# Optimization experiments

Measured on AMD Instinct MI355X. Metric: run time of the kernel, lower is better.

Reference implementation:

```python
import jax, jax.numpy as jnp
import numpy as np

B, S, D = 2, 2048, 1024
H = 16
HD = D // H  # 64
FORESIGHT = -1e9  # masked_fill value for non-causal positions


def setup_inputs() -> dict:
    key = jax.random.key(0)
    ks = jax.random.split(key, 8)
    s = 0.02
    return {
        "x": jax.random.normal(ks[0], (B, S, D), dtype=jnp.float32),
        "Wq": jax.random.normal(ks[1], (D, H * HD), dtype=jnp.float32) * s,
        "bq": jax.random.normal(ks[2], (H * HD,), dtype=jnp.float32) * s,
        "Wk": jax.random.normal(ks[3], (D, H * HD), dtype=jnp.float32) * s,
        "Wv": jax.random.normal(ks[4], (D, H * HD), dtype=jnp.float32) * s,
        "Wo": jax.random.normal(ks[5], (H * HD, D), dtype=jnp.float32) * s,
        "bo": jax.random.normal(ks[6], (D,), dtype=jnp.float32) * s,
    }


def reference(x, Wq, bq, Wk, Wv, Wo, bo):
    b, s, _ = x.shape
    # projections -> [B, H, S, HD]
    q = (x @ Wq + bq).reshape(b, s, H, HD).transpose(0, 2, 1, 3)
    k = (x @ Wk).reshape(b, s, H, HD).transpose(0, 2, 1, 3)
    v = (x @ Wv).reshape(b, s, H, HD).transpose(0, 2, 1, 3)
    # scores [B, H, S, S]
    scores = jnp.einsum("bhqd,bhkd->bhqk", q, k) / jnp.sqrt(jnp.float32(HD))
    # ALiBi bias: slope_h * j (key position), broadcast over queries
    slopes = 2.0 ** (-8.0 * jnp.arange(1, H + 1, dtype=jnp.float32) / H)
    positions = jnp.arange(s, dtype=jnp.float32)
    scores = scores - slopes[None, :, None, None] * positions[None, None, None, :]
    # causal mask: fill strictly-upper triangle with foresight
    causal = jnp.tril(jnp.ones((s, s), dtype=bool))
    scores = jnp.where(causal[None, None, :, :], scores, FORESIGHT)
    attn = jax.nn.softmax(scores, axis=-1)
    out = jnp.einsum("bhqk,bhkd->bhqd", attn, v)
    out = out.transpose(0, 2, 1, 3).reshape(b, s, H * HD)
    return out @ Wo + bo
```

## Files before the change

kernel.cpp:

```cpp
#include <hip/hip_runtime.h>
#include <stdint.h>

#define DDIM 1024
#define HH 16
#define HDIM 64
#define SS 2048

typedef short bf16x8 __attribute__((ext_vector_type(8)));
typedef short bf16x4 __attribute__((ext_vector_type(4)));
typedef float f32x4 __attribute__((ext_vector_type(4)));
typedef unsigned short u16;

__device__ __forceinline__ unsigned f2bf(float f) {
  unsigned u = __builtin_bit_cast(unsigned, f);
  u = u + 0x7FFFu + ((u >> 16) & 1u);
  return u >> 16;
}

__device__ __forceinline__ void mfma16(f32x4& c, bf16x4 a, bf16x4 b) {
  asm("v_mfma_f32_16x16x16_bf16 %0, %1, %2, %0" : "+v"(c) : "v"(a), "v"(b));
}

__device__ __forceinline__ void gload16(const void* g, void* l) {
  __builtin_amdgcn_global_load_lds(
      (const __attribute__((address_space(1))) unsigned int*)g,
      (__attribute__((address_space(3))) unsigned int*)l, 16, 0, 0);
}

__global__ void k_convert_x(const float* __restrict__ x, u16* __restrict__ xb) {
  int i = (blockIdx.x * 256 + threadIdx.x) * 4;
  float4 v = *(const float4*)(x + i);
  ushort4 o;
  o.x = (u16)f2bf(v.x); o.y = (u16)f2bf(v.y); o.z = (u16)f2bf(v.z); o.w = (u16)f2bf(v.w);
  *(ushort4*)(xb + i) = o;
}

__global__ void k_transpose_w(const float* __restrict__ w0, const float* __restrict__ w1,
                              const float* __restrict__ w2, const float* __restrict__ w3,
                              u16* __restrict__ wt) {
  __shared__ float t[64][65];
  int z = blockIdx.z;
  const float* src = (z == 0) ? w0 : (z == 1) ? w1 : (z == 2) ? w2 : w3;
  u16* dst = wt + (size_t)z * DDIM * DDIM;
  int k0 = blockIdx.x * 64, n0 = blockIdx.y * 64;
  int tid = threadIdx.x;
  int c4 = tid & 15, rr = tid >> 4;
  for (int rep = 0; rep < 4; rep++) {
    int r = rr + rep * 16;
    float4 v = *(const float4*)(src + (size_t)(k0 + r) * DDIM + n0 + c4 * 4);
    t[r][c4 * 4 + 0] = v.x; t[r][c4 * 4 + 1] = v.y;
    t[r][c4 * 4 + 2] = v.z; t[r][c4 * 4 + 3] = v.w;
  }
  __syncthreads();
  for (int rep = 0; rep < 4; rep++) {
    int n = rr + rep * 16;
    ushort4 o;
    o.x = (u16)f2bf(t[c4 * 4 + 0][n]); o.y = (u16)f2bf(t[c4 * 4 + 1][n]);
    o.z = (u16)f2bf(t[c4 * 4 + 2][n]); o.w = (u16)f2bf(t[c4 * 4 + 3][n]);
    *(ushort4*)(dst + (size_t)(n0 + n) * DDIM + k0 + c4 * 4) = o;
  }
}

template <int MODE>
__global__ __launch_bounds__(256, 2) void k_gemm(const u16* __restrict__ A,
                                                 const u16* __restrict__ BT,
                                                 const float* __restrict__ bias,
                                                 void* __restrict__ O0,
                                                 void* __restrict__ O1,
                                                 void* __restrict__ O2) {
  __shared__ __align__(16) u16 lA[128 * 64];
  __shared__ __align__(16) u16 lB[128 * 64];
  const int tid = threadIdx.x;
  const int l = tid & 63, w = tid >> 6;
  const int wm = w >> 1, wn = w & 1;
  const int m0 = blockIdx.x * 128, n0 = blockIdx.y * 128;
  const int lr = l >> 4, lc = l & 15;

  const int srow = l >> 3;
  const int scol = ((l & 7) ^ srow) * 8;

  f32x4 acc[4][4];
  for (int mi = 0; mi < 4; mi++)
    for (int ni = 0; ni < 4; ni++)
      acc[mi][ni] = f32x4{0.f, 0.f, 0.f, 0.f};

  for (int kk = 0; kk < 16; kk++) {
    const int k0 = kk * 64;
    for (int i = 0; i < 4; i++) {
      int c = w * 4 + i;
      gload16(A + (size_t)(m0 + c * 8 + srow) * DDIM + k0 + scol, (char*)lA + c * 1024);
      gload16(BT + (size_t)(n0 + c * 8 + srow) * DDIM + k0 + scol, (char*)lB + c * 1024);
    }
    __syncthreads();
    for (int ks = 0; ks < 2; ks++) {
      bf16x8 af[4], bfr[4];
      for (int mi = 0; mi < 4; mi++) {
        int row = wm * 64 + mi * 16 + lc;
        int slot = (ks * 4 + lr) ^ (row & 7);
        af[mi] = *(const bf16x8*)((const char*)lA + row * 128 + slot * 16);
      }
      for (int ni = 0; ni < 4; ni++) {
        int row = wn * 64 + ni * 16 + lc;
        int slot = (ks * 4 + lr) ^ (row & 7);
        bfr[ni] = *(const bf16x8*)((const char*)lB + row * 128 + slot * 16);
      }
      for (int mi = 0; mi < 4; mi++)
        for (int ni = 0; ni < 4; ni++)
          acc[mi][ni] = __builtin_amdgcn_mfma_f32_16x16x32_bf16(af[mi], bfr[ni], acc[mi][ni], 0, 0, 0);
    }
    __syncthreads();
  }

  if (MODE == 0) {
    const int which = blockIdx.y >> 3;
    if (which == 0) {
      u16* C = (u16*)O0;
      for (int mi = 0; mi < 4; mi++)
        for (int ni = 0; ni < 4; ni++) {
          int nl = (n0 + wn * 64 + ni * 16 + lc) & 1023;
          float badd = bias[nl];
          for (int r = 0; r < 4; r++) {
            int m = m0 + wm * 64 + mi * 16 + lr * 4 + r;
            C[(size_t)m * DDIM + nl] = (u16)f2bf(acc[mi][ni][r] + badd);
          }
        }
    } else if (which == 1) {
      u16* C = (u16*)O1;
      for (int mi = 0; mi < 4; mi++)
        for (int ni = 0; ni < 4; ni++) {
          int nl = (n0 + wn * 64 + ni * 16 + lc) & 1023;
          for (int r = 0; r < 4; r++) {
            int m = m0 + wm * 64 + mi * 16 + lr * 4 + r;
            C[(size_t)m * DDIM + nl] = (u16)f2bf(acc[mi][ni][r]);
          }
        }
    } else {
      u16* C = (u16*)O2;
      for (int mi = 0; mi < 4; mi++)
        for (int ni = 0; ni < 4; ni++) {
          int nl = (n0 + wn * 64 + ni * 16 + lc) & 1023;
          int h = nl >> 6, hd = nl & 63;
          int m = m0 + wm * 64 + mi * 16 + lr * 4;
          int b = m >> 11, s = m & 2047;
          unsigned d0 = f2bf(acc[mi][ni][0]) | (f2bf(acc[mi][ni][1]) << 16);
          unsigned d1 = f2bf(acc[mi][ni][2]) | (f2bf(acc[mi][ni][3]) << 16);
          u16* p = C + ((size_t)((b * HH + h) * HDIM + hd)) * SS + s;
          *(unsigned*)(p) = d0;
          *(unsigned*)(p + 2) = d1;
        }
    }
  } else {
    float* C = (float*)O0;
    for (int mi = 0; mi < 4; mi++)
      for (int ni = 0; ni < 4; ni++) {
        int n = n0 + wn * 64 + ni * 16 + lc;
        float badd = bias[n];
        for (int r = 0; r < 4; r++) {
          int m = m0 + wm * 64 + mi * 16 + lr * 4 + r;
          C[(size_t)m * DDIM + n] = acc[mi][ni][r] + badd;
        }
      }
  }
}

__device__ __forceinline__ void attn_tile(int kt, bool masked, int kfhi,
                                          const char* lKc, const char* lVc,
                                          const bf16x8 qf[2], f32x4 of[4],
                                          float& mrun, float& lrun,
                                          float slope, int lr, int lc, int q_glob) {
  f32x4 sf[8];
#pragma unroll
  for (int kf = 0; kf < 8; kf++) sf[kf] = f32x4{0.f, 0.f, 0.f, 0.f};
#pragma unroll
  for (int ks = 0; ks < 2; ks++)
#pragma unroll
    for (int kf = 0; kf < 8; kf++) {
      if (kf >= kfhi) continue;
      int key = kf * 16 + lc;
      int slot = (ks * 4 + lr) ^ (lc & 7);
      bf16x8 a = *(const bf16x8*)(lKc + key * 128 + slot * 16);
      sf[kf] = __builtin_amdgcn_mfma_f32_16x16x32_bf16(a, qf[ks], sf[kf], 0, 0, 0);
    }

  float tmax = -INFINITY;
#pragma unroll
  for (int kf = 0; kf < 8; kf++) {
    if (kf >= kfhi) continue;
#pragma unroll
    for (int r = 0; r < 4; r++) {
      int key = kt * 128 + kf * 16 + lr * 4 + r;
      float sv = sf[kf][r] * 0.125f - slope * (float)key;
      if (masked && key > q_glob) sv = -1e9f;
      sf[kf][r] = sv;
      tmax = fmaxf(tmax, sv);
    }
  }
  tmax = fmaxf(tmax, __shfl_xor(tmax, 16));
  tmax = fmaxf(tmax, __shfl_xor(tmax, 32));

  if (tmax > mrun) {
    float corr = __expf(mrun - tmax);
    lrun *= corr;
#pragma unroll
    for (int mf = 0; mf < 4; mf++) {
      of[mf][0] *= corr; of[mf][1] *= corr; of[mf][2] *= corr; of[mf][3] *= corr;
    }
    mrun = tmax;
  }

  f32x4 ps = f32x4{0.f, 0.f, 0.f, 0.f};
  bf16x4 pb[8];
#pragma unroll
  for (int kf = 0; kf < 8; kf++) {
    if (kf >= kfhi) continue;
    unsigned a0 = f2bf(__expf(sf[kf][0] - mrun));
    unsigned a1 = f2bf(__expf(sf[kf][1] - mrun));
    unsigned a2 = f2bf(__expf(sf[kf][2] - mrun));
    unsigned a3 = f2bf(__expf(sf[kf][3] - mrun));
    uint2 uu;
    uu.x = a0 | (a1 << 16);
    uu.y = a2 | (a3 << 16);
    pb[kf] = __builtin_bit_cast(bf16x4, uu);
    ps[0] += __builtin_bit_cast(float, a0 << 16);
    ps[1] += __builtin_bit_cast(float, a1 << 16);
    ps[2] += __builtin_bit_cast(float, a2 << 16);
    ps[3] += __builtin_bit_cast(float, a3 << 16);
  }
  float psum = (ps[0] + ps[1]) + (ps[2] + ps[3]);
  psum += __shfl_xor(psum, 16);
  psum += __shfl_xor(psum, 32);
  lrun += psum;

#pragma unroll
  for (int kf = 0; kf < 8; kf++) {
    if (kf >= kfhi) continue;
    int g2 = (kf << 1) + (lr >> 1);
#pragma unroll
    for (int mf = 0; mf < 4; mf++) {
      int hd = mf * 16 + lc;
      int byte = hd * 256 + ((g2 ^ (hd & 7)) << 4) + ((lr & 1) << 3);
      bf16x4 va = *(const bf16x4*)(lVc + byte);
      mfma16(of[mf], va, pb[kf]);
    }
  }
}

__global__ __launch_bounds__(256, 4) void k_attn(const u16* __restrict__ Q,
                                                 const u16* __restrict__ Kg,
                                                 const u16* __restrict__ Vt,
                                                 u16* __restrict__ AO) {
  __shared__ __align__(16) u16 lK[128 * 64];
  __shared__ __align__(16) u16 lV[64 * 128];

  const int tid = threadIdx.x;
  const int l = tid & 63, w = tid >> 6;
  const int lr = l >> 4, lc = l & 15;
  const int bh = blockIdx.x;
  const int b = bh >> 4, h = bh & 15;
  const int yq = blockIdx.y;
  const int fk = yq & 7, fj = yq >> 3;
  const int qt = (fj == 0) ? fk : (fj == 1) ? (15 - fk) : (fj == 2) ? (16 + fk) : (31 - fk);

  const float slope = exp2f(-0.5f * (float)(h + 1));
  const int q_glob = qt * 64 + w * 16 + lc;

  bf16x8 qf[2];
#pragma unroll
  for (int ks = 0; ks < 2; ks++)
    qf[ks] = *(const bf16x8*)(Q + (size_t)(b * SS + q_glob) * DDIM + h * HDIM + ks * 32 + lr * 8);

  f32x4 of[4];
#pragma unroll
  for (int mf = 0; mf < 4; mf++) of[mf] = f32x4{0.f, 0.f, 0.f, 0.f};
  float mrun = -INFINITY, lrun = 0.f;

  const int srowK = l >> 3;
  const int scolK = ((l & 7) ^ srowK) * 8;
  const int nkt = qt / 2 + 1;

  auto stage = [&](int kt) {
#pragma unroll
    for (int i = 0; i < 4; i++) {
      int c = w * 4 + i;
      gload16(Kg + (size_t)(b * SS + kt * 128 + c * 8 + srowK) * DDIM + h * HDIM + scolK,
              (char*)lK + c * 1024);
      int hd = c * 4 + lr;
      gload16(Vt + ((size_t)bh * HDIM + hd) * SS + kt * 128 + (((l & 15) ^ (hd & 7)) << 3),
              (char*)lV + c * 1024);
    }
  };

  for (int kt = 0; kt < nkt - 1; kt++) {
    stage(kt);
    __syncthreads();
    attn_tile(kt, false, 8, (const char*)lK, (const char*)lV, qf, of, mrun, lrun,
              slope, lr, lc, q_glob);
    __syncthreads();
  }
  stage(nkt - 1);
  __syncthreads();
  if (qt & 1)
    attn_tile(nkt - 1, true, 8, (const char*)lK, (const char*)lV, qf, of, mrun, lrun,
              slope, lr, lc, q_glob);
  else
    attn_tile(nkt - 1, true, 4, (const char*)lK, (const char*)lV, qf, of, mrun, lrun,
              slope, lr, lc, q_glob);

  float inv = 1.f / lrun;
  u16* obase = AO + (size_t)(b * SS + q_glob) * DDIM + h * HDIM;
#pragma unroll
  for (int mf = 0; mf < 4; mf++) {
    uint2 uu;
    uu.x = f2bf(of[mf][0] * inv) | (f2bf(of[mf][1] * inv) << 16);
    uu.y = f2bf(of[mf][2] * inv) | (f2bf(of[mf][3] * inv) << 16);
    *(uint2*)(obase + mf * 16 + lr * 4) = uu;
  }
}

extern "C" void kernel_launch(void* const* d_in, const int* in_sizes, int n_in,
                              void* d_out, int out_size, void* d_ws, size_t ws_size,
                              hipStream_t stream) {
  const float* x  = (const float*)d_in[0];
  const float* Wq = (const float*)d_in[1];
  const float* bq = (const float*)d_in[2];
  const float* Wk = (const float*)d_in[3];
  const float* Wv = (const float*)d_in[4];
  const float* Wo = (const float*)d_in[5];
  const float* bo = (const float*)d_in[6];
  float* out = (float*)d_out;

  u16* ws = (u16*)d_ws;
  const size_t MEG = 1024 * 1024;
  u16* xb = ws;
  u16* WT = ws + 4 * MEG;
  u16* Qb = ws + 8 * MEG;
  u16* Kb = ws + 12 * MEG;
  u16* Vt = ws + 16 * MEG;
  u16* AO = ws + 20 * MEG;

  k_convert_x<<<dim3(4096), dim3(256), 0, stream>>>(x, xb);
  k_transpose_w<<<dim3(16, 16, 4), dim3(256), 0, stream>>>(Wq, Wk, Wv, Wo, WT);
  k_gemm<0><<<dim3(32, 24), dim3(256), 0, stream>>>(xb, WT, bq, (void*)Qb, (void*)Kb, (void*)Vt);
  k_attn<<<dim3(32, 32), dim3(256), 0, stream>>>(Qb, Kb, Vt, AO);
  k_gemm<1><<<dim3(32, 8), dim3(256), 0, stream>>>(AO, WT + 3 * MEG, bo, (void*)out, nullptr, nullptr);
}
```

Before: 123.7 us.

## Fold softmax scale into Q, use exp2 softmax, packed bf16 converts, setprio, remap grid

The Q projection epilogue now multiplies by 0.125*log2(e), so the attention kernel can use exp2 with a pre-scaled ALiBi slope and drop the per-element score scaling. Manual bf16 rounding is replaced with the hardware v_cvt_pk_bf16_f32 instruction, and the row sum is taken from the fp32 probabilities instead of the rounded values. s_setprio is raised around the MFMA sections. The attention grid becomes 1D, with query tiles paired short/long inside each batch-head, which changes block scheduling order and load balance. The sum change introduces small numeric differences.

```diff
diff --git a/kernel.cpp b/kernel.cpp
--- a/kernel.cpp
+++ b/kernel.cpp
@@ -15,6 +15,12 @@
   unsigned u = __builtin_bit_cast(unsigned, f);
   u = u + 0x7FFFu + ((u >> 16) & 1u);
   return u >> 16;
+}
+
+__device__ __forceinline__ unsigned cvt_pk_bf16(float a, float b) {
+  unsigned r;
+  asm("v_cvt_pk_bf16_f32 %0, %1, %2" : "=v"(r) : "v"(a), "v"(b));
+  return r;
 }
 
 __device__ __forceinline__ void mfma16(f32x4& c, bf16x4 a, bf16x4 b) {
@@ -115,13 +121,14 @@
     const int which = blockIdx.y >> 3;
     if (which == 0) {
       u16* C = (u16*)O0;
+      const float c1 = 0.18033688011112043f;
       for (int mi = 0; mi < 4; mi++)
         for (int ni = 0; ni < 4; ni++) {
           int nl = (n0 + wn * 64 + ni * 16 + lc) & 1023;
           float badd = bias[nl];
           for (int r = 0; r < 4; r++) {
             int m = m0 + wm * 64 + mi * 16 + lr * 4 + r;
-            C[(size_t)m * DDIM + nl] = (u16)f2bf(acc[mi][ni][r] + badd);
+            C[(size_t)m * DDIM + nl] = (u16)f2bf((acc[mi][ni][r] + badd) * c1);
           }
         }
     } else if (which == 1) {
@@ -167,10 +174,11 @@
                                           const char* lKc, const char* lVc,
                                           const bf16x8 qf[2], f32x4 of[4],
                                           float& mrun, float& lrun,
-                                          float slope, int lr, int lc, int q_glob) {
+                                          float slope2, int lr, int lc, int q_glob) {
   f32x4 sf[8];
 #pragma unroll
   for (int kf = 0; kf < 8; kf++) sf[kf] = f32x4{0.f, 0.f, 0.f, 0.f};
+  __builtin_amdgcn_s_setprio(1);
 #pragma unroll
   for (int ks = 0; ks < 2; ks++)
 #pragma unroll
@@ -181,16 +189,20 @@
       bf16x8 a = *(const bf16x8*)(lKc + key * 128 + slot * 16);
       sf[kf] = __builtin_amdgcn_mfma_f32_16x16x32_bf16(a, qf[ks], sf[kf], 0, 0, 0);
     }
-
-  float tmax = -INFINITY;
+  __builtin_amdgcn_s_setprio(0);
+
+  const float kbase = -slope2 * (float)(kt * 128 + lr * 4);
+  float tmax = -3.0e38f;
 #pragma unroll
   for (int kf = 0; kf < 8; kf++) {
     if (kf >= kfhi) continue;
 #pragma unroll
     for (int r = 0; r < 4; r++) {
-      int key = kt * 128 + kf * 16 + lr * 4 + r;
-      float sv = sf[kf][r] * 0.125f - slope * (float)key;
-      if (masked && key > q_glob) sv = -1e9f;
+      float sv = sf[kf][r] + (kbase - slope2 * (float)(kf * 16 + r));
+      if (masked) {
+        int key = kt * 128 + kf * 16 + lr * 4 + r;
+        if (key > q_glob) sv = -3.0e38f;
+      }
       sf[kf][r] = sv;
       tmax = fmaxf(tmax, sv);
     }
@@ -199,7 +211,7 @@
   tmax = fmaxf(tmax, __shfl_xor(tmax, 32));
 
   if (tmax > mrun) {
-    float corr = __expf(mrun - tmax);
+    float corr = exp2f(mrun - tmax);
     lrun *= corr;
 #pragma unroll
     for (int mf = 0; mf < 4; mf++) {
@@ -213,24 +225,22 @@
 #pragma unroll
   for (int kf = 0; kf < 8; kf++) {
     if (kf >= kfhi) continue;
-    unsigned a0 = f2bf(__expf(sf[kf][0] - mrun));
-    unsigned a1 = f2bf(__expf(sf[kf][1] - mrun));
-    unsigned a2 = f2bf(__expf(sf[kf][2] - mrun));
-    unsigned a3 = f2bf(__expf(sf[kf][3] - mrun));
+    float p0 = exp2f(sf[kf][0] - mrun);
+    float p1 = exp2f(sf[kf][1] - mrun);
+    float p2 = exp2f(sf[kf][2] - mrun);
+    float p3 = exp2f(sf[kf][3] - mrun);
+    ps[0] += p0; ps[1] += p1; ps[2] += p2; ps[3] += p3;
     uint2 uu;
-    uu.x = a0 | (a1 << 16);
-    uu.y = a2 | (a3 << 16);
+    uu.x = cvt_pk_bf16(p0, p1);
+    uu.y = cvt_pk_bf16(p2, p3);
     pb[kf] = __builtin_bit_cast(bf16x4, uu);
-    ps[0] += __builtin_bit_cast(float, a0 << 16);
-    ps[1] += __builtin_bit_cast(float, a1 << 16);
-    ps[2] += __builtin_bit_cast(float, a2 << 16);
-    ps[3] += __builtin_bit_cast(float, a3 << 16);
   }
   float psum = (ps[0] + ps[1]) + (ps[2] + ps[3]);
   psum += __shfl_xor(psum, 16);
   psum += __shfl_xor(psum, 32);
   lrun += psum;
 
+  __builtin_amdgcn_s_setprio(1);
 #pragma unroll
   for (int kf = 0; kf < 8; kf++) {
     if (kf >= kfhi) continue;
@@ -243,6 +253,7 @@
       mfma16(of[mf], va, pb[kf]);
     }
   }
+  __builtin_amdgcn_s_setprio(0);
 }
 
 __global__ __launch_bounds__(256, 4) void k_attn(const u16* __restrict__ Q,
@@ -255,13 +266,14 @@
   const int tid = threadIdx.x;
   const int l = tid & 63, w = tid >> 6;
   const int lr = l >> 4, lc = l & 15;
-  const int bh = blockIdx.x;
+  const int id = blockIdx.x;
+  const int bh = id >> 5;
+  const int p5 = id & 31;
+  const int kq = p5 >> 1;
+  const int qt = (p5 & 1) ? (31 - kq) : kq;
   const int b = bh >> 4, h = bh & 15;
-  const int yq = blockIdx.y;
-  const int fk = yq & 7, fj = yq >> 3;
-  const int qt = (fj == 0) ? fk : (fj == 1) ? (15 - fk) : (fj == 2) ? (16 + fk) : (31 - fk);
-
-  const float slope = exp2f(-0.5f * (float)(h + 1));
+
+  const float slope2 = exp2f(-0.5f * (float)(h + 1)) * 1.4426950408889634f;
   const int q_glob = qt * 64 + w * 16 + lc;
 
   bf16x8 qf[2];
@@ -272,7 +284,7 @@
   f32x4 of[4];
 #pragma unroll
   for (int mf = 0; mf < 4; mf++) of[mf] = f32x4{0.f, 0.f, 0.f, 0.f};
-  float mrun = -INFINITY, lrun = 0.f;
+  float mrun = -3.0e38f, lrun = 0.f;
 
   const int srowK = l >> 3;
   const int scolK = ((l & 7) ^ srowK) * 8;
@@ -294,25 +306,25 @@
     stage(kt);
     __syncthreads();
     attn_tile(kt, false, 8, (const char*)lK, (const char*)lV, qf, of, mrun, lrun,
-              slope, lr, lc, q_glob);
+              slope2, lr, lc, q_glob);
     __syncthreads();
   }
   stage(nkt - 1);
   __syncthreads();
   if (qt & 1)
     attn_tile(nkt - 1, true, 8, (const char*)lK, (const char*)lV, qf, of, mrun, lrun,
-              slope, lr, lc, q_glob);
+              slope2, lr, lc, q_glob);
   else
     attn_tile(nkt - 1, true, 4, (const char*)lK, (const char*)lV, qf, of, mrun, lrun,
-              slope, lr, lc, q_glob);
+              slope2, lr, lc, q_glob);
 
   float inv = 1.f / lrun;
   u16* obase = AO + (size_t)(b * SS + q_glob) * DDIM + h * HDIM;
 #pragma unroll
   for (int mf = 0; mf < 4; mf++) {
     uint2 uu;
-    uu.x = f2bf(of[mf][0] * inv) | (f2bf(of[mf][1] * inv) << 16);
-    uu.y = f2bf(of[mf][2] * inv) | (f2bf(of[mf][3] * inv) << 16);
+    uu.x = cvt_pk_bf16(of[mf][0] * inv, of[mf][1] * inv);
+    uu.y = cvt_pk_bf16(of[mf][2] * inv, of[mf][3] * inv);
     *(uint2*)(obase + mf * 16 + lr * 4) = uu;
   }
 }
@@ -341,6 +353,6 @@
   k_convert_x<<<dim3(4096), dim3(256), 0, stream>>>(x, xb);
   k_transpose_w<<<dim3(16, 16, 4), dim3(256), 0, stream>>>(Wq, Wk, Wv, Wo, WT);
   k_gemm<0><<<dim3(32, 24), dim3(256), 0, stream>>>(xb, WT, bq, (void*)Qb, (void*)Kb, (void*)Vt);
-  k_attn<<<dim3(32, 32), dim3(256), 0, stream>>>(Qb, Kb, Vt, AO);
+  k_attn<<<dim3(1024), dim3(256), 0, stream>>>(Qb, Kb, Vt, AO);
   k_gemm<1><<<dim3(32, 8), dim3(256), 0, stream>>>(AO, WT + 3 * MEG, bo, (void*)out, nullptr, nullptr);
 }
```

New measurement: 141.7 us. +14.6%, slower.
